# Kernel tuning notes

Hardware: AMD Instinct MI355X
Metric: run time of the kernel (lower is better)

Reference implementation:

```python
import jax, jax.numpy as jnp
import numpy as np

KEY_CH = 256

def _conv1x1(w, b, t):
    # 1x1 conv with BN folded: t [B,Cin,N] -> [B,Cout,N]
    return jnp.einsum('oc,bcn->bon', w, t) + b[None, :, None]

def _conv1x1_relu(w, b, t):
    return jax.nn.relu(_conv1x1(w, b, t))

def setup_inputs() -> dict:
    key = jax.random.key(0)
    ks = jax.random.split(key, 12)
    B, C, H, W = 4, 512, 128, 128
    d = {}
    d['feat'] = jax.random.normal(ks[0], (B, C, H, W), jnp.float32)
    d['prob'] = jax.random.normal(ks[1], (B, 20, H, W), jnp.float32)  # unused by forward (overwritten)
    s = 0.02
    d['wp1'] = jax.random.normal(ks[2], (KEY_CH, C), jnp.float32) * s
    d['bp1'] = jnp.zeros((KEY_CH,), jnp.float32)
    d['wp2'] = jax.random.normal(ks[3], (KEY_CH, KEY_CH), jnp.float32) * s
    d['bp2'] = jnp.zeros((KEY_CH,), jnp.float32)
    d['wo1'] = jax.random.normal(ks[4], (KEY_CH, C), jnp.float32) * s
    d['bo1'] = jnp.zeros((KEY_CH,), jnp.float32)
    d['wo2'] = jax.random.normal(ks[5], (KEY_CH, KEY_CH), jnp.float32) * s
    d['bo2'] = jnp.zeros((KEY_CH,), jnp.float32)
    d['wd'] = jax.random.normal(ks[6], (KEY_CH, C), jnp.float32) * s
    d['bd'] = jnp.zeros((KEY_CH,), jnp.float32)
    d['wu'] = jax.random.normal(ks[7], (C, KEY_CH), jnp.float32) * s
    d['bu'] = jnp.zeros((C,), jnp.float32)
    d['wout'] = jax.random.normal(ks[8], (512, 2 * C), jnp.float32) * s
    d['bout'] = jnp.zeros((512,), jnp.float32)
    return d


def reference(feat, prob, wp1, bp1, wp2, bp2, wo1, bo1, wo2, bo2, wd, bd, wu, bu, wout, bout):
    B, C, H, W = feat.shape
    x = feat.reshape(B, C, H * W)  # [B,C,N]
    # prob = upsample_bilinear(feat, (H,W)) == feat (identity resize); prob arg is dead.
    # SpatialGather (scale=1): softmax over spatial, weighted pool of features.
    pw = jax.nn.softmax(x, axis=-1)                     # [B,K,N], K == C here
    context = jnp.einsum('bkn,bcn->bck', pw, x)         # [B,C,K] proxy features
    # ObjectAttentionBlock2D
    q = _conv1x1_relu(wp2, bp2, _conv1x1_relu(wp1, bp1, x))        # [B,key,N]
    k = _conv1x1_relu(wo2, bo2, _conv1x1_relu(wo1, bo1, context))  # [B,key,K]
    v = _conv1x1_relu(wd, bd, context)                             # [B,key,K]
    sim = jnp.einsum('bdn,bdk->bnk', q, k) * (KEY_CH ** -0.5)      # [B,N,K]
    sim = jax.nn.softmax(sim, axis=-1)
    ctx = jnp.einsum('bnk,bdk->bdn', sim, v)                       # [B,key,N]
    ctx = _conv1x1_relu(wu, bu, ctx)                               # [B,C,N]
    # SpatialOCR: concat + 1x1 conv + BN + ReLU (dropout identity at eval)
    out = _conv1x1_relu(wout, bout, jnp.concatenate([ctx, x], axis=1))  # [B,out,N]
    return out.reshape(B, -1, H, W)
```

## Files before the change

### kernel.cpp

```cpp
#include <hip/hip_runtime.h>

typedef unsigned int u32;
typedef unsigned short u16;
typedef short s16x8 __attribute__((ext_vector_type(8)));
typedef float f32x4 __attribute__((ext_vector_type(4)));

__device__ __forceinline__ u16 f2bf(float f) {
  u32 u = __float_as_uint(f);
  u32 r = (u + 0x7fffu + ((u >> 16) & 1u)) >> 16;
  return (u16)r;
}

template <int MODE>
__device__ __forceinline__ uint4 pack8(const float* p, float2 st) {
  float4 f0 = *(const float4*)p;
  float4 f1 = *(const float4*)(p + 4);
  float v[8] = {f0.x, f0.y, f0.z, f0.w, f1.x, f1.y, f1.z, f1.w};
  if (MODE == 2) {
#pragma unroll
    for (int j = 0; j < 8; ++j) v[j] = __expf(v[j] - st.x) * st.y;
  }
  uint4 o;
  o.x = (u32)f2bf(v[0]) | ((u32)f2bf(v[1]) << 16);
  o.y = (u32)f2bf(v[2]) | ((u32)f2bf(v[3]) << 16);
  o.z = (u32)f2bf(v[4]) | ((u32)f2bf(v[5]) << 16);
  o.w = (u32)f2bf(v[6]) | ((u32)f2bf(v[7]) << 16);
  return o;
}

__device__ __forceinline__ void g2l16(u16* lds, const u16* g) {
  __builtin_amdgcn_global_load_lds(
      (const __attribute__((address_space(1))) void*)g,
      (__attribute__((address_space(3))) void*)lds, 16, 0, 0);
}

__global__ __launch_bounds__(256) void row_softmax_bf16(
    const float* __restrict__ feat, u16* __restrict__ expx,
    u16* __restrict__ xbf) {
  const long long row = blockIdx.x;
  const float* xp = feat + row * 16384;
  const int tid = threadIdx.x, wv = tid >> 6, ln = tid & 63;
  __shared__ float red[4];
  float4 v[16];
  float mx = -1e30f;
#pragma unroll
  for (int p = 0; p < 16; ++p) {
    v[p] = *(const float4*)(xp + tid * 4 + p * 1024);
    mx = fmaxf(mx, fmaxf(fmaxf(v[p].x, v[p].y), fmaxf(v[p].z, v[p].w)));
  }
  u16* bp = xbf + row * 16384;
#pragma unroll
  for (int p = 0; p < 16; ++p) {
    uint2 ow;
    ow.x = (u32)f2bf(v[p].x) | ((u32)f2bf(v[p].y) << 16);
    ow.y = (u32)f2bf(v[p].z) | ((u32)f2bf(v[p].w) << 16);
    *(uint2*)(bp + tid * 4 + p * 1024) = ow;
  }
  for (int o = 32; o; o >>= 1) mx = fmaxf(mx, __shfl_xor(mx, o, 64));
  if (!ln) red[wv] = mx;
  __syncthreads();
  mx = fmaxf(fmaxf(red[0], red[1]), fmaxf(red[2], red[3]));
  __syncthreads();
  float s = 0.f;
#pragma unroll
  for (int p = 0; p < 16; ++p) {
    v[p].x = __expf(v[p].x - mx);
    v[p].y = __expf(v[p].y - mx);
    v[p].z = __expf(v[p].z - mx);
    v[p].w = __expf(v[p].w - mx);
    s += v[p].x + v[p].y + v[p].z + v[p].w;
  }
  for (int o = 32; o; o >>= 1) s += __shfl_xor(s, o, 64);
  if (!ln) red[wv] = s;
  __syncthreads();
  const float inv = 1.f / (red[0] + red[1] + red[2] + red[3]);
  u16* op = expx + row * 16384;
#pragma unroll
  for (int p = 0; p < 16; ++p) {
    uint2 ow;
    ow.x = (u32)f2bf(v[p].x * inv) | ((u32)f2bf(v[p].y * inv) << 16);
    ow.y = (u32)f2bf(v[p].z * inv) | ((u32)f2bf(v[p].w * inv) << 16);
    *(uint2*)(op + tid * 4 + p * 1024) = ow;
  }
}

__global__ __launch_bounds__(256) void transpose_x(const u16* __restrict__ xbf,
                                                   u16* __restrict__ catT) {
  __shared__ u16 t[32][33];
  const int b = blockIdx.z;
  const int c0 = blockIdx.y << 5, n0 = blockIdx.x << 5;
  const int tx = threadIdx.x & 31, ty = threadIdx.x >> 5;
  const u16* fb = xbf + (long long)b * 512 * 16384;
#pragma unroll
  for (int i = 0; i < 32; i += 8)
    t[ty + i][tx] = fb[(long long)(c0 + ty + i) * 16384 + n0 + tx];
  __syncthreads();
  u16* ob = catT + (long long)b * 16384 * 1024 + 512;
#pragma unroll
  for (int i = 0; i < 32; i += 8)
    ob[(long long)(n0 + ty + i) * 1024 + c0 + tx] = t[tx][ty + i];
}

__global__ __launch_bounds__(256) void cvt_weights(
    const float* __restrict__ w0, const float* __restrict__ w1,
    const float* __restrict__ w2, const float* __restrict__ w3,
    const float* __restrict__ w4, const float* __restrict__ w5,
    const float* __restrict__ w6, u16* __restrict__ dst) {
  const long long i = (long long)blockIdx.x * 256 + threadIdx.x;
  const float* s;
  long long off;
  if (i < 131072) { s = w0; off = 0; }
  else if (i < 196608) { s = w1; off = 131072; }
  else if (i < 327680) { s = w2; off = 196608; }
  else if (i < 393216) { s = w3; off = 327680; }
  else if (i < 524288) { s = w4; off = 393216; }
  else if (i < 655360) { s = w5; off = 524288; }
  else { s = w6; off = 655360; }
  dst[i] = f2bf(s[i - off]);
}

template <int ACT, int BIAS, int SPLITK, int F32OUT>
__global__ __launch_bounds__(512, 1) void gemm256_nt(
    const u16* __restrict__ A, long long sA, int lda,
    const u16* __restrict__ B, long long sB, int ldb,
    void* __restrict__ C, long long sC, int ldc,
    const float* __restrict__ bias, int K, int kchunk) {
  __shared__ __align__(16) u16 As[2][256 * 64];
  __shared__ __align__(16) u16 Bs[2][256 * 64];
  const int tid = threadIdx.x;
  const int wid = tid >> 6, ln = tid & 63;
  const int bz = blockIdx.z;
  const int batch = SPLITK ? (bz >> SPLITK) : bz;
  const int chunk = SPLITK ? (bz & ((1 << SPLITK) - 1)) : 0;
  const long long tm = (long long)blockIdx.y << 8;
  const long long tn = (long long)blockIdx.x << 8;
  const int srow = wid * 8 + (ln >> 3);
  const int scl = ((ln & 7) ^ (ln >> 3)) << 3;
  const long long koff = SPLITK ? (long long)chunk * kchunk : 0;
  const u16* Ab = A + (long long)batch * sA + koff + scl;
  const u16* Bb = B + (long long)batch * sB + koff + scl;
  const u16* rA[4];
  const u16* rB[4];
#pragma unroll
  for (int s = 0; s < 4; ++s) {
    rA[s] = Ab + (tm + s * 64 + srow) * (long long)lda;
    rB[s] = Bb + (tn + s * 64 + srow) * (long long)ldb;
  }
  auto stage = [&](int buf, int kk) {
#pragma unroll
    for (int s = 0; s < 4; ++s) {
      g2l16(&As[buf][s * 4096 + wid * 512], rA[s] + kk);
      g2l16(&Bs[buf][s * 4096 + wid * 512], rB[s] + kk);
    }
  };
  const int fr = ln & 15, fq = ln >> 4;
  const int wm8 = wid >> 2;
  const int wn8 = wid & 3;
  const int arow = (wm8 * 128 + fr) * 64;
  const int brow = (wn8 * 64 + fr) * 64;
  const int ax = fr & 7;
  const int c0 = ((fq ^ ax) << 3);
  const int c1 = c0 ^ 32;
  f32x4 acc[8][4] = {};
  const int nt = (SPLITK ? kchunk : K) >> 6;
  stage(0, 0);
  if (nt > 1) stage(1, 64);
  for (int kt = 0; kt < nt; ++kt) {
    const int cur = kt & 1;
    if (kt + 1 < nt)
      asm volatile("s_waitcnt vmcnt(8)" ::: "memory");
    else
      asm volatile("s_waitcnt vmcnt(0)" ::: "memory");
    asm volatile("s_barrier" ::: "memory");
    s16x8 bfr[4][2], afr[8][2];
#pragma unroll
    for (int nf = 0; nf < 4; ++nf) {
      bfr[nf][0] = *(const s16x8*)&Bs[cur][brow + nf * 1024 + c0];
      bfr[nf][1] = *(const s16x8*)&Bs[cur][brow + nf * 1024 + c1];
    }
#pragma unroll
    for (int mf = 0; mf < 8; ++mf) {
      afr[mf][0] = *(const s16x8*)&As[cur][arow + mf * 1024 + c0];
      afr[mf][1] = *(const s16x8*)&As[cur][arow + mf * 1024 + c1];
    }
    __builtin_amdgcn_sched_barrier(0);
    asm volatile("s_waitcnt lgkmcnt(0)" ::: "memory");
    asm volatile("s_barrier" ::: "memory");
    if (kt + 2 < nt) stage(cur, (kt + 2) << 6);
    __builtin_amdgcn_sched_barrier(0);
    __builtin_amdgcn_s_setprio(1);
#pragma unroll
    for (int mf = 0; mf < 8; ++mf)
#pragma unroll
      for (int nf = 0; nf < 4; ++nf) {
        acc[mf][nf] = __builtin_amdgcn_mfma_f32_16x16x32_bf16(
            afr[mf][0], bfr[nf][0], acc[mf][nf], 0, 0, 0);
        acc[mf][nf] = __builtin_amdgcn_mfma_f32_16x16x32_bf16(
            afr[mf][1], bfr[nf][1], acc[mf][nf], 0, 0, 0);
      }
    __builtin_amdgcn_s_setprio(0);
  }
#pragma unroll
  for (int mf = 0; mf < 8; ++mf) {
    const long long gr0 = tm + wm8 * 128 + mf * 16 + fq * 4;
#pragma unroll
    for (int nf = 0; nf < 4; ++nf) {
      const long long gc = tn + wn8 * 64 + nf * 16 + fr;
      float bc = 0.f;
      if (BIAS == 2) bc = bias[gc];
#pragma unroll
      for (int t = 0; t < 4; ++t) {
        float v = acc[mf][nf][t];
        if (BIAS == 1) v += bias[gr0 + t];
        if (BIAS == 2) v += bc;
        if (ACT) v = fmaxf(v, 0.f);
        const long long idx = (long long)batch * sC + (gr0 + t) * ldc + gc;
        if (SPLITK)
          atomicAdd((float*)C + idx, v);
        else if (F32OUT)
          ((float*)C)[idx] = v;
        else
          ((u16*)C)[idx] = f2bf(v);
      }
    }
  }
}

template <int ACT, int BIAS, int SPLITK, int AMODE, int BMODE, int F32OUT>
__global__ __launch_bounds__(256, 4) void gemm_nt(
    const void* __restrict__ Av, long long sA, int lda,
    const void* __restrict__ Bv, long long sB, int ldb,
    void* __restrict__ C, long long sC, int ldc,
    const float* __restrict__ bias, int K, int kchunk,
    const float2* __restrict__ stats, int statsStride) {
  __shared__ __align__(16) u16 Asm_[2][128 * 32];
  __shared__ __align__(16) u16 Bsm_[2][128 * 32];
  const int tid = threadIdx.x;
  const int wv = tid >> 6;
  const int ln = tid & 63;
  const int bz = blockIdx.z;
  const int batch = SPLITK ? (bz >> 3) : bz;
  const int chunk = SPLITK ? (bz & 7) : 0;
  const long long tm = (long long)blockIdx.y << 7;
  const long long tn = (long long)blockIdx.x << 7;
  const int lrow = ln >> 2;
  const int lcol = (((ln & 3) ^ ((ln >> 3) & 3)) << 3);
  const int w32 = wv << 5;
  const long long ar0 = tm + w32 + lrow, ar1 = ar0 + 16;
  const long long br0 = tn + w32 + lrow, br1 = br0 + 16;
  const long long koff = (long long)chunk * kchunk + lcol;
  const u16* gau0 = (const u16*)Av + (long long)batch * sA + koff + ar0 * lda;
  const u16* gau1 = (const u16*)Av + (long long)batch * sA + koff + ar1 * lda;
  const u16* gbu0 = (const u16*)Bv + (long long)batch * sB + koff + br0 * ldb;
  const u16* gbu1 = (const u16*)Bv + (long long)batch * sB + koff + br1 * ldb;
  const int fr = ln & 15;
  const int fq = ln >> 4;
  const int wm = (wv >> 1) << 6;
  const int wn = (wv & 1) << 6;
  const int rx = (fq ^ ((fr >> 1) & 3)) << 3;
  f32x4 acc[4][4] = {};
  auto stage = [&](int bo, int kk) {
    g2l16(&Asm_[0][bo + w32 * 32], gau0 + kk);
    g2l16(&Asm_[0][bo + w32 * 32 + 512], gau1 + kk);
    g2l16(&Bsm_[0][bo + w32 * 32], gbu0 + kk);
    g2l16(&Bsm_[0][bo + w32 * 32 + 512], gbu1 + kk);
  };
  stage(0, 0);
  asm volatile("s_waitcnt vmcnt(0)" ::: "memory");
  asm volatile("s_barrier" ::: "memory");
  int cb = 0;
  for (int kk = 0; kk < K; kk += 32) {
    s16x8 af[4], bfr[4];
#pragma unroll
    for (int i = 0; i < 4; ++i)
      af[i] = *(const s16x8*)&Asm_[0][cb + (wm + i * 16 + fr) * 32 + rx];
#pragma unroll
    for (int j = 0; j < 4; ++j)
      bfr[j] = *(const s16x8*)&Bsm_[0][cb + (wn + j * 16 + fr) * 32 + rx];
    if (kk + 32 < K) stage(cb ^ 4096, kk + 32);
#pragma unroll
    for (int i = 0; i < 4; ++i)
#pragma unroll
      for (int j = 0; j < 4; ++j)
        acc[i][j] = __builtin_amdgcn_mfma_f32_16x16x32_bf16(
            af[i], bfr[j], acc[i][j], 0, 0, 0);
    __builtin_amdgcn_sched_barrier(0);
    asm volatile("s_waitcnt vmcnt(0) lgkmcnt(0)" ::: "memory");
    asm volatile("s_barrier" ::: "memory");
    cb ^= 4096;
  }
#pragma unroll
  for (int i = 0; i < 4; ++i) {
    const long long gr0 = tm + wm + i * 16 + fq * 4;
#pragma unroll
    for (int j = 0; j < 4; ++j) {
      const long long gc = tn + wn + j * 16 + fr;
      float bc = 0.f;
      if (BIAS == 2) bc = bias[gc];
#pragma unroll
      for (int t = 0; t < 4; ++t) {
        float v = acc[i][j][t];
        if (BIAS == 1) v += bias[gr0 + t];
        if (BIAS == 2) v += bc;
        if (ACT) v = fmaxf(v, 0.f);
        const long long idx = (long long)batch * sC + (gr0 + t) * ldc + gc;
        if (SPLITK)
          atomicAdd((float*)C + idx, v);
        else if (F32OUT)
          ((float*)C)[idx] = v;
        else
          ((u16*)C)[idx] = f2bf(v);
      }
    }
  }
}

__global__ __launch_bounds__(256) void cvt_f32_bf16(const float* __restrict__ s,
                                                    u16* __restrict__ d) {
  const int i = blockIdx.x * 256 + threadIdx.x;
  d[i] = f2bf(s[i]);
}

__global__ __launch_bounds__(256) void softmax_p(u16* __restrict__ P) {
  const int wv = threadIdx.x >> 6, ln = threadIdx.x & 63;
  const long long row = (long long)blockIdx.x * 4 + wv;
  u16* rp = P + row * 1024;
  uint4 r = *(const uint4*)(rp + ln * 8);
  u32 w[4] = {r.x, r.y, r.z, r.w};
  float v[8];
#pragma unroll
  for (int k = 0; k < 4; ++k) {
    v[2 * k] = __uint_as_float(w[k] << 16) * 0.0625f;
    v[2 * k + 1] = __uint_as_float(w[k] & 0xffff0000u) * 0.0625f;
  }
  float m = v[0];
#pragma unroll
  for (int t = 1; t < 8; ++t) m = fmaxf(m, v[t]);
  for (int o = 32; o; o >>= 1) m = fmaxf(m, __shfl_xor(m, o, 64));
  float e[8], s = 0.f;
#pragma unroll
  for (int t = 0; t < 8; ++t) {
    e[t] = __expf(v[t] - m);
    s += e[t];
  }
  for (int o = 32; o; o >>= 1) s += __shfl_xor(s, o, 64);
  const float inv = 1.f / s;
  u32 ow[4];
#pragma unroll
  for (int k = 0; k < 4; ++k)
    ow[k] = (u32)f2bf(e[2 * k] * inv) | ((u32)f2bf(e[2 * k + 1] * inv) << 16);
  *(uint4*)(rp + ln * 8) = make_uint4(ow[0], ow[1], ow[2], ow[3]);
}

extern "C" void kernel_launch(void* const* d_in, const int* in_sizes, int n_in,
                              void* d_out, int out_size, void* d_ws, size_t ws_size,
                              hipStream_t stream) {
  const float* feat = (const float*)d_in[0];
  const float* wp1 = (const float*)d_in[2];
  const float* bp1 = (const float*)d_in[3];
  const float* wp2 = (const float*)d_in[4];
  const float* bp2 = (const float*)d_in[5];
  const float* wo1 = (const float*)d_in[6];
  const float* bo1 = (const float*)d_in[7];
  const float* wo2 = (const float*)d_in[8];
  const float* bo2 = (const float*)d_in[9];
  const float* wd = (const float*)d_in[10];
  const float* bd = (const float*)d_in[11];
  const float* wu = (const float*)d_in[12];
  const float* bu = (const float*)d_in[13];
  const float* wout = (const float*)d_in[14];
  const float* bout = (const float*)d_in[15];
  float* outp = (float*)d_out;
  char* ws = (char*)d_ws;

  u16* catT = (u16*)ws;
  u16* expx = (u16*)(ws + 134217728LL);
  u16* q1T = (u16*)(ws + 134217728LL);
  u16* ctxT = q1T;
  u16* qT = (u16*)(ws + 167772160LL);
  float* ctxF = (float*)(ws + 201326592LL);
  u16* wb = (u16*)(ws + 201326592LL);
  u16* conT = (u16*)(ws + 205520896LL);
  u16* k1hT = (u16*)(ws + 207618048LL);
  u16* kTm = (u16*)(ws + 208666624LL);
  u16* vm = (u16*)(ws + 209715200LL);
  if (ws_size < 210763776ULL) return;
  u16* xbf = (u16*)d_out;
  u16* wp1b = wb + 0;
  u16* wp2b = wb + 131072;
  u16* wo1b = wb + 196608;
  u16* wo2b = wb + 327680;
  u16* wdb = wb + 393216;
  u16* wub = wb + 524288;
  u16* woutb = wb + 655360;

  row_softmax_bf16<<<2048, 256, 0, stream>>>(feat, expx, xbf);
  transpose_x<<<dim3(512, 16, 4), 256, 0, stream>>>(xbf, catT);
  hipMemsetAsync(ctxF, 0, 4194304, stream);
  gemm256_nt<0, 0, 4, 0><<<dim3(2, 2, 64), 512, 0, stream>>>(
      expx, 8388608LL, 16384, xbf, 8388608LL, 16384, ctxF, 262144LL, 512,
      nullptr, 16384, 1024);
  cvt_f32_bf16<<<4096, 256, 0, stream>>>(ctxF, conT);
  cvt_weights<<<4608, 256, 0, stream>>>(wp1, wp2, wo1, wo2, wd, wu, wout, wb);
  gemm_nt<1, 2, 0, 0, 0, 0><<<dim3(2, 4, 4), 256, 0, stream>>>(
      conT, 262144LL, 512, wo1b, 0LL, 512, k1hT, 131072LL, 256, bo1, 512, 0,
      nullptr, 0);
  gemm_nt<1, 2, 0, 0, 0, 0><<<dim3(2, 4, 4), 256, 0, stream>>>(
      k1hT, 131072LL, 256, wo2b, 0LL, 256, kTm, 131072LL, 256, bo2, 256, 0,
      nullptr, 0);
  gemm_nt<1, 1, 0, 0, 0, 0><<<dim3(4, 2, 4), 256, 0, stream>>>(
      wdb, 0LL, 512, conT, 262144LL, 512, vm, 131072LL, 512, bd, 512, 0,
      nullptr, 0);
  gemm256_nt<1, 2, 0, 0><<<dim3(1, 64, 4), 512, 0, stream>>>(
      catT + 512, 16777216LL, 1024, wp1b, 0LL, 512, q1T, 4194304LL, 256, bp1,
      512, 0);
  gemm256_nt<1, 2, 0, 0><<<dim3(1, 64, 4), 512, 0, stream>>>(
      q1T, 4194304LL, 256, wp2b, 0LL, 256, qT, 4194304LL, 256, bp2, 256, 0);
  gemm256_nt<0, 0, 0, 0><<<dim3(2, 64, 4), 512, 0, stream>>>(
      qT, 4194304LL, 256, kTm, 131072LL, 256, catT, 16777216LL, 1024, nullptr,
      256, 0);
  softmax_p<<<16384, 256, 0, stream>>>(catT);
  gemm256_nt<0, 0, 0, 0><<<dim3(1, 64, 4), 512, 0, stream>>>(
      catT, 16777216LL, 1024, vm, 131072LL, 512, ctxT, 4194304LL, 256, nullptr,
      512, 0);
  gemm256_nt<1, 2, 0, 0><<<dim3(2, 64, 4), 512, 0, stream>>>(
      ctxT, 4194304LL, 256, wub, 0LL, 256, catT, 16777216LL, 1024, bu, 256, 0);
  gemm256_nt<1, 1, 0, 1><<<dim3(64, 2, 4), 512, 0, stream>>>(
      woutb, 0LL, 1024, catT, 16777216LL, 1024, outp, 8388608LL, 16384, bout,
      1024, 0);
}
```

Baseline: 645.5 us.

## Replace split-K atomics with per-chunk stores plus reduction; interleave LDS loads with MFMA

```diff
diff --git a/kernel.cpp b/kernel.cpp
--- a/kernel.cpp
+++ b/kernel.cpp
@@ -9,23 +9,6 @@
   u32 u = __float_as_uint(f);
   u32 r = (u + 0x7fffu + ((u >> 16) & 1u)) >> 16;
   return (u16)r;
-}
-
-template <int MODE>
-__device__ __forceinline__ uint4 pack8(const float* p, float2 st) {
-  float4 f0 = *(const float4*)p;
-  float4 f1 = *(const float4*)(p + 4);
-  float v[8] = {f0.x, f0.y, f0.z, f0.w, f1.x, f1.y, f1.z, f1.w};
-  if (MODE == 2) {
-#pragma unroll
-    for (int j = 0; j < 8; ++j) v[j] = __expf(v[j] - st.x) * st.y;
-  }
-  uint4 o;
-  o.x = (u32)f2bf(v[0]) | ((u32)f2bf(v[1]) << 16);
-  o.y = (u32)f2bf(v[2]) | ((u32)f2bf(v[3]) << 16);
-  o.z = (u32)f2bf(v[4]) | ((u32)f2bf(v[5]) << 16);
-  o.w = (u32)f2bf(v[6]) | ((u32)f2bf(v[7]) << 16);
-  return o;
 }
 
 __device__ __forceinline__ void g2l16(u16* lds, const u16* g) {
@@ -119,7 +102,7 @@
   dst[i] = f2bf(s[i - off]);
 }
 
-template <int ACT, int BIAS, int SPLITK, int F32OUT>
+template <int ACT, int BIAS, int SPLITK, int F32OUT, int SPLITOUT>
 __global__ __launch_bounds__(512, 1) void gemm256_nt(
     const u16* __restrict__ A, long long sA, int lda,
     const u16* __restrict__ B, long long sB, int ldb,
@@ -172,7 +155,8 @@
     else
       asm volatile("s_waitcnt vmcnt(0)" ::: "memory");
     asm volatile("s_barrier" ::: "memory");
-    s16x8 bfr[4][2], afr[8][2];
+    __builtin_amdgcn_s_setprio(1);
+    s16x8 bfr[4][2];
 #pragma unroll
     for (int nf = 0; nf < 4; ++nf) {
       bfr[nf][0] = *(const s16x8*)&Bs[cur][brow + nf * 1024 + c0];
@@ -180,25 +164,20 @@
     }
 #pragma unroll
     for (int mf = 0; mf < 8; ++mf) {
-      afr[mf][0] = *(const s16x8*)&As[cur][arow + mf * 1024 + c0];
-      afr[mf][1] = *(const s16x8*)&As[cur][arow + mf * 1024 + c1];
+      s16x8 a0 = *(const s16x8*)&As[cur][arow + mf * 1024 + c0];
+      s16x8 a1 = *(const s16x8*)&As[cur][arow + mf * 1024 + c1];
+#pragma unroll
+      for (int nf = 0; nf < 4; ++nf) {
+        acc[mf][nf] = __builtin_amdgcn_mfma_f32_16x16x32_bf16(
+            a0, bfr[nf][0], acc[mf][nf], 0, 0, 0);
+        acc[mf][nf] = __builtin_amdgcn_mfma_f32_16x16x32_bf16(
+            a1, bfr[nf][1], acc[mf][nf], 0, 0, 0);
+      }
     }
-    __builtin_amdgcn_sched_barrier(0);
+    __builtin_amdgcn_s_setprio(0);
     asm volatile("s_waitcnt lgkmcnt(0)" ::: "memory");
     asm volatile("s_barrier" ::: "memory");
     if (kt + 2 < nt) stage(cur, (kt + 2) << 6);
-    __builtin_amdgcn_sched_barrier(0);
-    __builtin_amdgcn_s_setprio(1);
-#pragma unroll
-    for (int mf = 0; mf < 8; ++mf)
-#pragma unroll
-      for (int nf = 0; nf < 4; ++nf) {
-        acc[mf][nf] = __builtin_amdgcn_mfma_f32_16x16x32_bf16(
-            afr[mf][0], bfr[nf][0], acc[mf][nf], 0, 0, 0);
-        acc[mf][nf] = __builtin_amdgcn_mfma_f32_16x16x32_bf16(
-            afr[mf][1], bfr[nf][1], acc[mf][nf], 0, 0, 0);
-      }
-    __builtin_amdgcn_s_setprio(0);
   }
 #pragma unroll
   for (int mf = 0; mf < 8; ++mf) {
@@ -214,10 +193,12 @@
         if (BIAS == 1) v += bias[gr0 + t];
         if (BIAS == 2) v += bc;
         if (ACT) v = fmaxf(v, 0.f);
-        const long long idx = (long long)batch * sC + (gr0 + t) * ldc + gc;
-        if (SPLITK)
+        const long long cslot = (SPLITK && SPLITOUT) ? (long long)bz
+                                                     : (long long)batch;
+        const long long idx = cslot * sC + (gr0 + t) * ldc + gc;
+        if (SPLITK && !SPLITOUT)
           atomicAdd((float*)C + idx, v);
-        else if (F32OUT)
+        else if (F32OUT || SPLITOUT)
           ((float*)C)[idx] = v;
         else
           ((u16*)C)[idx] = f2bf(v);
@@ -226,7 +207,7 @@
   }
 }
 
-template <int ACT, int BIAS, int SPLITK, int AMODE, int BMODE, int F32OUT>
+template <int ACT, int BIAS, int AMODE, int BMODE, int F32OUT>
 __global__ __launch_bounds__(256, 4) void gemm_nt(
     const void* __restrict__ Av, long long sA, int lda,
     const void* __restrict__ Bv, long long sB, int ldb,
@@ -238,9 +219,7 @@
   const int tid = threadIdx.x;
   const int wv = tid >> 6;
   const int ln = tid & 63;
-  const int bz = blockIdx.z;
-  const int batch = SPLITK ? (bz >> 3) : bz;
-  const int chunk = SPLITK ? (bz & 7) : 0;
+  const int batch = blockIdx.z;
   const long long tm = (long long)blockIdx.y << 7;
   const long long tn = (long long)blockIdx.x << 7;
   const int lrow = ln >> 2;
@@ -248,7 +227,7 @@
   const int w32 = wv << 5;
   const long long ar0 = tm + w32 + lrow, ar1 = ar0 + 16;
   const long long br0 = tn + w32 + lrow, br1 = br0 + 16;
-  const long long koff = (long long)chunk * kchunk + lcol;
+  const long long koff = lcol;
   const u16* gau0 = (const u16*)Av + (long long)batch * sA + koff + ar0 * lda;
   const u16* gau1 = (const u16*)Av + (long long)batch * sA + koff + ar1 * lda;
   const u16* gbu0 = (const u16*)Bv + (long long)batch * sB + koff + br0 * ldb;
@@ -304,9 +283,7 @@
         if (BIAS == 2) v += bc;
         if (ACT) v = fmaxf(v, 0.f);
         const long long idx = (long long)batch * sC + (gr0 + t) * ldc + gc;
-        if (SPLITK)
-          atomicAdd((float*)C + idx, v);
-        else if (F32OUT)
+        if (F32OUT)
           ((float*)C)[idx] = v;
         else
           ((u16*)C)[idx] = f2bf(v);
@@ -315,10 +292,21 @@
   }
 }
 
-__global__ __launch_bounds__(256) void cvt_f32_bf16(const float* __restrict__ s,
-                                                    u16* __restrict__ d) {
+__global__ __launch_bounds__(256) void reduce16_bf16(const float* __restrict__ s,
+                                                     u16* __restrict__ d) {
   const int i = blockIdx.x * 256 + threadIdx.x;
-  d[i] = f2bf(s[i]);
+  const int b = i >> 16, w = i & 65535;
+  const float4* base = (const float4*)s + (long long)b * 16 * 65536 + w;
+  float4 a = base[0];
+#pragma unroll
+  for (int c = 1; c < 16; ++c) {
+    float4 t = base[(long long)c * 65536];
+    a.x += t.x; a.y += t.y; a.z += t.z; a.w += t.w;
+  }
+  uint2 ow;
+  ow.x = (u32)f2bf(a.x) | ((u32)f2bf(a.y) << 16);
+  ow.y = (u32)f2bf(a.z) | ((u32)f2bf(a.w) << 16);
+  *(uint2*)(d + (long long)i * 4) = ow;
 }
 
 __global__ __launch_bounds__(256) void softmax_p(u16* __restrict__ P) {
@@ -378,7 +366,6 @@
   u16* q1T = (u16*)(ws + 134217728LL);
   u16* ctxT = q1T;
   u16* qT = (u16*)(ws + 167772160LL);
-  float* ctxF = (float*)(ws + 201326592LL);
   u16* wb = (u16*)(ws + 201326592LL);
   u16* conT = (u16*)(ws + 205520896LL);
   u16* k1hT = (u16*)(ws + 207618048LL);
@@ -386,6 +373,7 @@
   u16* vm = (u16*)(ws + 209715200LL);
   if (ws_size < 210763776ULL) return;
   u16* xbf = (u16*)d_out;
+  float* ctxChunks = (float*)((char*)d_out + 67108864LL);
   u16* wp1b = wb + 0;
   u16* wp2b = wb + 131072;
   u16* wo1b = wb + 196608;
@@ -396,36 +384,35 @@
 
   row_softmax_bf16<<<2048, 256, 0, stream>>>(feat, expx, xbf);
   transpose_x<<<dim3(512, 16, 4), 256, 0, stream>>>(xbf, catT);
-  hipMemsetAsync(ctxF, 0, 4194304, stream);
-  gemm256_nt<0, 0, 4, 0><<<dim3(2, 2, 64), 512, 0, stream>>>(
-      expx, 8388608LL, 16384, xbf, 8388608LL, 16384, ctxF, 262144LL, 512,
+  gemm256_nt<0, 0, 4, 1, 1><<<dim3(2, 2, 64), 512, 0, stream>>>(
+      expx, 8388608LL, 16384, xbf, 8388608LL, 16384, ctxChunks, 262144LL, 512,
       nullptr, 16384, 1024);
-  cvt_f32_bf16<<<4096, 256, 0, stream>>>(ctxF, conT);
+  reduce16_bf16<<<1024, 256, 0, stream>>>(ctxChunks, conT);
   cvt_weights<<<4608, 256, 0, stream>>>(wp1, wp2, wo1, wo2, wd, wu, wout, wb);
-  gemm_nt<1, 2, 0, 0, 0, 0><<<dim3(2, 4, 4), 256, 0, stream>>>(
+  gemm_nt<1, 2, 0, 0, 0><<<dim3(2, 4, 4), 256, 0, stream>>>(
       conT, 262144LL, 512, wo1b, 0LL, 512, k1hT, 131072LL, 256, bo1, 512, 0,
       nullptr, 0);
-  gemm_nt<1, 2, 0, 0, 0, 0><<<dim3(2, 4, 4), 256, 0, stream>>>(
+  gemm_nt<1, 2, 0, 0, 0><<<dim3(2, 4, 4), 256, 0, stream>>>(
       k1hT, 131072LL, 256, wo2b, 0LL, 256, kTm, 131072LL, 256, bo2, 256, 0,
       nullptr, 0);
-  gemm_nt<1, 1, 0, 0, 0, 0><<<dim3(4, 2, 4), 256, 0, stream>>>(
+  gemm_nt<1, 1, 0, 0, 0><<<dim3(4, 2, 4), 256, 0, stream>>>(
       wdb, 0LL, 512, conT, 262144LL, 512, vm, 131072LL, 512, bd, 512, 0,
       nullptr, 0);
-  gemm256_nt<1, 2, 0, 0><<<dim3(1, 64, 4), 512, 0, stream>>>(
+  gemm256_nt<1, 2, 0, 0, 0><<<dim3(1, 64, 4), 512, 0, stream>>>(
       catT + 512, 16777216LL, 1024, wp1b, 0LL, 512, q1T, 4194304LL, 256, bp1,
       512, 0);
-  gemm256_nt<1, 2, 0, 0><<<dim3(1, 64, 4), 512, 0, stream>>>(
+  gemm256_nt<1, 2, 0, 0, 0><<<dim3(1, 64, 4), 512, 0, stream>>>(
       q1T, 4194304LL, 256, wp2b, 0LL, 256, qT, 4194304LL, 256, bp2, 256, 0);
-  gemm256_nt<0, 0, 0, 0><<<dim3(2, 64, 4), 512, 0, stream>>>(
+  gemm256_nt<0, 0, 0, 0, 0><<<dim3(2, 64, 4), 512, 0, stream>>>(
       qT, 4194304LL, 256, kTm, 131072LL, 256, catT, 16777216LL, 1024, nullptr,
       256, 0);
   softmax_p<<<16384, 256, 0, stream>>>(catT);
-  gemm256_nt<0, 0, 0, 0><<<dim3(1, 64, 4), 512, 0, stream>>>(
+  gemm256_nt<0, 0, 0, 0, 0><<<dim3(1, 64, 4), 512, 0, stream>>>(
       catT, 16777216LL, 1024, vm, 131072LL, 512, ctxT, 4194304LL, 256, nullptr,
       512, 0);
-  gemm256_nt<1, 2, 0, 0><<<dim3(2, 64, 4), 512, 0, stream>>>(
+  gemm256_nt<1, 2, 0, 0, 0><<<dim3(2, 64, 4), 512, 0, stream>>>(
       ctxT, 4194304LL, 256, wub, 0LL, 256, catT, 16777216LL, 1024, bu, 256, 0);
-  gemm256_nt<1, 1, 0, 1><<<dim3(64, 2, 4), 512, 0, stream>>>(
+  gemm256_nt<1, 1, 0, 1, 0><<<dim3(64, 2, 4), 512, 0, stream>>>(
       woutb, 0LL, 1024, catT, 16777216LL, 1024, outp, 8388608LL, 16384, bout,
       1024, 0);
 }
```

Measured after the change: 648.4 us. About the same (+0.4%).
